# Kernel tuning notes

Measured on AMD Instinct MI355X. Metric: run time of the kernel, lower is better.

The kernel has to match this reference:

```python
import jax, jax.numpy as jnp
import numpy as np
import math

D_MODEL = 512
NHEAD = 8
HEAD = D_MODEL // NHEAD


def _pe(length, d):
    pos = np.arange(length)[:, None].astype(np.float32)
    div = np.exp(np.arange(0, d, 2).astype(np.float32) * (-math.log(10000.0) / d))
    pe = np.zeros((length, d), np.float32)
    pe[:, 0::2] = np.sin(pos * div)
    pe[:, 1::2] = np.cos(pos * div)
    return jnp.asarray(pe)


def _ln(x, g, b, eps=1e-5):
    m = x.mean(-1, keepdims=True)
    v = ((x - m) ** 2).mean(-1, keepdims=True)
    return (x - m) / jnp.sqrt(v + eps) * g + b


def _mha(q_in, k_in, v_in, w_in, b_in, w_out, b_out, mask=None):
    d = q_in.shape[-1]
    wq, wk, wv = jnp.split(w_in, 3, axis=0)
    bq, bk, bv = jnp.split(b_in, 3, axis=0)
    B, Sq, _ = q_in.shape
    Sk = k_in.shape[1]
    q = (q_in @ wq.T + bq).reshape(B, Sq, NHEAD, HEAD)
    k = (k_in @ wk.T + bk).reshape(B, Sk, NHEAD, HEAD)
    v = (v_in @ wv.T + bv).reshape(B, Sk, NHEAD, HEAD)
    s = jnp.einsum('bqhd,bkhd->bhqk', q, k) / math.sqrt(HEAD)
    if mask is not None:
        s = s + mask
    a = jax.nn.softmax(s, axis=-1)
    o = jnp.einsum('bhqk,bkhd->bqhd', a, v).reshape(B, Sq, d)
    return o @ w_out.T + b_out


def setup_inputs() -> dict:
    rng = np.random.default_rng(0)
    def r(*s):
        return jnp.asarray(rng.standard_normal(s, dtype=np.float32) * 0.02)
    L, d, ff, di, do = 6, 512, 2048, 64, 64
    B, S, T = 4, 512, 256
    return dict(
        src=jnp.asarray(rng.standard_normal((B, S, di), dtype=np.float32)),
        tgt=jnp.asarray(rng.standard_normal((B, T, do), dtype=np.float32)),
        enc_in_w=r(d, di), enc_in_b=r(d),
        dec_in_w=r(d, do), dec_in_b=r(d),
        out_w=r(do, d), out_b=r(do),
        enc_attn_w=r(L, 3 * d, d), enc_attn_b=r(L, 3 * d),
        enc_out_w=r(L, d, d), enc_out_b=r(L, d),
        enc_ff1_w=r(L, ff, d), enc_ff1_b=r(L, ff),
        enc_ff2_w=r(L, d, ff), enc_ff2_b=r(L, d),
        enc_ln1_g=jnp.ones((L, d)), enc_ln1_b=jnp.zeros((L, d)),
        enc_ln2_g=jnp.ones((L, d)), enc_ln2_b=jnp.zeros((L, d)),
        dec_sa_w=r(L, 3 * d, d), dec_sa_b=r(L, 3 * d),
        dec_sa_out_w=r(L, d, d), dec_sa_out_b=r(L, d),
        dec_ca_w=r(L, 3 * d, d), dec_ca_b=r(L, 3 * d),
        dec_ca_out_w=r(L, d, d), dec_ca_out_b=r(L, d),
        dec_ff1_w=r(L, ff, d), dec_ff1_b=r(L, ff),
        dec_ff2_w=r(L, d, ff), dec_ff2_b=r(L, d),
        dec_ln1_g=jnp.ones((L, d)), dec_ln1_b=jnp.zeros((L, d)),
        dec_ln2_g=jnp.ones((L, d)), dec_ln2_b=jnp.zeros((L, d)),
        dec_ln3_g=jnp.ones((L, d)), dec_ln3_b=jnp.zeros((L, d)),
    )


def reference(src, tgt, enc_in_w, enc_in_b, dec_in_w, dec_in_b, out_w, out_b,
              enc_attn_w, enc_attn_b, enc_out_w, enc_out_b,
              enc_ff1_w, enc_ff1_b, enc_ff2_w, enc_ff2_b,
              enc_ln1_g, enc_ln1_b, enc_ln2_g, enc_ln2_b,
              dec_sa_w, dec_sa_b, dec_sa_out_w, dec_sa_out_b,
              dec_ca_w, dec_ca_b, dec_ca_out_w, dec_ca_out_b,
              dec_ff1_w, dec_ff1_b, dec_ff2_w, dec_ff2_b,
              dec_ln1_g, dec_ln1_b, dec_ln2_g, dec_ln2_b, dec_ln3_g, dec_ln3_b):
    d = D_MODEL
    sq = math.sqrt(d)
    S, T = src.shape[1], tgt.shape[1]
    L = enc_attn_w.shape[0]
    # encoder: 'cosine' pos encoding (dropout disabled / eval)
    x = (src @ enc_in_w.T + enc_in_b) * sq + _pe(S, d)[None]
    for i in range(L):
        a = _mha(x, x, x, enc_attn_w[i], enc_attn_b[i], enc_out_w[i], enc_out_b[i])
        x = _ln(x + a, enc_ln1_g[i], enc_ln1_b[i])
        f = jax.nn.relu(x @ enc_ff1_w[i].T + enc_ff1_b[i]) @ enc_ff2_w[i].T + enc_ff2_b[i]
        x = _ln(x + f, enc_ln2_g[i], enc_ln2_b[i])
    memory = x
    # decoder: teacher-forced prefix loop == single causal-masked pass.
    # NOTE: original adds pe[0] to EVERY step (pos_encoder on a length-1 slice).
    y = (tgt @ dec_in_w.T + dec_in_b) * sq + _pe(1, d)[0]
    mask = jnp.where(jnp.tril(jnp.ones((T, T), bool)), 0.0, -1e9).astype(y.dtype)
    for i in range(L):
        a = _mha(y, y, y, dec_sa_w[i], dec_sa_b[i], dec_sa_out_w[i], dec_sa_out_b[i], mask)
        y = _ln(y + a, dec_ln1_g[i], dec_ln1_b[i])
        c = _mha(y, memory, memory, dec_ca_w[i], dec_ca_b[i], dec_ca_out_w[i], dec_ca_out_b[i])
        y = _ln(y + c, dec_ln2_g[i], dec_ln2_b[i])
        f = jax.nn.relu(y @ dec_ff1_w[i].T + dec_ff1_b[i]) @ dec_ff2_w[i].T + dec_ff2_b[i]
        y = _ln(y + f, dec_ln3_g[i], dec_ln3_b[i])
    return y @ out_w.T + out_b
```

## Files before the change

kernel.cpp:

```cpp
#include <hip/hip_runtime.h>
#include <hip/hip_bf16.h>
#include <math.h>

#define BB 4
#define SEQ 512
#define TGT 256
#define DM 512
#define FFD 2048
#define NH 8
#define HD 64
#define NL 6

typedef unsigned short u16;
typedef __attribute__((ext_vector_type(4))) float f4;
typedef __attribute__((ext_vector_type(4))) unsigned short us4;
typedef __attribute__((ext_vector_type(8))) unsigned short us8;
typedef __attribute__((ext_vector_type(8))) short s8;

__device__ inline u16 f2b(float f) {
    __hip_bfloat16 h = __float2bfloat16(f);
    return *reinterpret_cast<u16*>(&h);
}
__device__ inline float b2f(u16 u) {
    unsigned int x = ((unsigned int)u) << 16;
    float f;
    __builtin_memcpy(&f, &x, 4);
    return f;
}
__device__ inline us4 cvt4(f4 v) {
    us4 u;
    u.x = f2b(v.x); u.y = f2b(v.y); u.z = f2b(v.z); u.w = f2b(v.w);
    return u;
}

struct CastSegs {
    const float* src[24];
    u16* dst[24];
    int cum[25];
    int nseg;
};

__global__ __launch_bounds__(256) void castseg_k(CastSegs cs)
{
    const int g0 = blockIdx.x << 10;
    int s = 0;
    while (g0 >= cs.cum[s + 1]) s++;
    const f4* __restrict__ sp = (const f4*)cs.src[s];
    us8* __restrict__ dp = (us8*)cs.dst[s];
    const int base = g0 - cs.cum[s] + (int)threadIdx.x;

    f4 lo[4], hi[4];
#pragma unroll
    for (int k = 0; k < 4; k++) {
        size_t g = (size_t)(base + (k << 8));
        lo[k] = sp[g * 2];
        hi[k] = sp[g * 2 + 1];
    }
#pragma unroll
    for (int k = 0; k < 4; k++) {
        us4 ul = cvt4(lo[k]), uh = cvt4(hi[k]);
        us8 o;
#pragma unroll
        for (int e = 0; e < 4; e++) { o[e] = ul[e]; o[e + 4] = uh[e]; }
        dp[base + (k << 8)] = o;
    }
}

__global__ void kvbias_k(const float* __restrict__ dec_ca_b, float* __restrict__ out)
{
    int idx = blockIdx.x * blockDim.x + threadIdx.x;
    if (idx >= NL * 2 * DM) return;
    int layer = idx >> 10, j = idx & 1023;
    out[idx] = dec_ca_b[layer * 3 * DM + DM + j];
}

template <int RELU, int OUTF32, int BM, int PE>
__global__ __launch_bounds__(256) void mgemm_k(
    const u16* __restrict__ A, const u16* __restrict__ W,
    const float* __restrict__ bias, const u16* __restrict__ resid,
    void* __restrict__ Cv, int M, int N, int K, float alpha)
{
    constexpr int MI = BM / 32;
    __shared__ u16 As[2][BM][72];
    __shared__ u16 Bs[2][64][72];
    const int bm = blockIdx.y * BM, bn = blockIdx.x * 64;
    const int tid = threadIdx.x;
    const int wave = tid >> 6, lane = tid & 63;
    const int wr = (wave >> 1) * (BM / 2), wc = (wave & 1) * 32;
    const int lm = lane & 15, quad = lane >> 4;
    const int sbr = tid >> 2, sbc = (tid & 3) * 16;
    const int sar = (BM == 64) ? (tid >> 2) : (tid >> 3);
    const int sac = (BM == 64) ? ((tid & 3) * 16) : ((tid & 7) * 8);

    const u16* Arow = A + (size_t)(bm + sar) * K + sac;
    const u16* Wrow = W + (size_t)(bn + sbr) * K + sbc;

    us8 a0 = *(const us8*)(Arow);
    us8 a1;
    if (BM == 64) a1 = *(const us8*)(Arow + 8);
    us8 b0 = *(const us8*)(Wrow);
    us8 b1 = *(const us8*)(Wrow + 8);

    f4 acc[MI][2];
#pragma unroll
    for (int i = 0; i < MI; i++)
#pragma unroll
        for (int j = 0; j < 2; j++) acc[i][j] = (f4)(0.f);

    const int nk = K >> 6;
    *(us8*)&As[0][sar][sac] = a0;
    if (BM == 64) *(us8*)&As[0][sar][sac + 8] = a1;
    *(us8*)&Bs[0][sbr][sbc] = b0;
    *(us8*)&Bs[0][sbr][sbc + 8] = b1;
    __syncthreads();

    for (int t = 0; t < nk; t++) {
        const int cb = t & 1;
        if (t + 1 < nk) {
            int off = (t + 1) << 6;
            a0 = *(const us8*)(Arow + off);
            if (BM == 64) a1 = *(const us8*)(Arow + off + 8);
            b0 = *(const us8*)(Wrow + off);
            b1 = *(const us8*)(Wrow + off + 8);
        }
#pragma unroll
        for (int ks = 0; ks < 2; ks++) {
            s8 af[MI], bfr[2];
#pragma unroll
            for (int i = 0; i < MI; i++) af[i] = *(const s8*)&As[cb][wr + i * 16 + lm][ks * 32 + quad * 8];
#pragma unroll
            for (int j = 0; j < 2; j++) bfr[j] = *(const s8*)&Bs[cb][wc + j * 16 + lm][ks * 32 + quad * 8];
#pragma unroll
            for (int i = 0; i < MI; i++)
#pragma unroll
                for (int j = 0; j < 2; j++)
                    acc[i][j] = __builtin_amdgcn_mfma_f32_16x16x32_bf16(af[i], bfr[j], acc[i][j], 0, 0, 0);
        }
        if (t + 1 < nk) {
            const int nb = cb ^ 1;
            *(us8*)&As[nb][sar][sac] = a0;
            if (BM == 64) *(us8*)&As[nb][sar][sac + 8] = a1;
            *(us8*)&Bs[nb][sbr][sbc] = b0;
            *(us8*)&Bs[nb][sbr][sbc + 8] = b1;
            __syncthreads();
        }
    }

#pragma unroll
    for (int j = 0; j < 2; j++) {
        int n = bn + wc + j * 16 + lm;
        float bv = bias[n];
        float dv = 0.f;
        if (PE == 1) dv = expf((float)(n & ~1) * (-9.210340371976184f / (float)DM));
#pragma unroll
        for (int i = 0; i < MI; i++) {
#pragma unroll
            for (int r = 0; r < 4; r++) {
                int m = bm + wr + i * 16 + quad * 4 + r;
                float v = (acc[i][j][r] + bv) * alpha;
                if (PE == 1) {
                    float ang = (float)(m & (SEQ - 1)) * dv;
                    v += (n & 1) ? cosf(ang) : sinf(ang);
                }
                if (PE == 2) { if (n & 1) v += 1.f; }
                if (RELU) v = fmaxf(v, 0.f);
                size_t off = (size_t)m * N + n;
                if (resid) v += b2f(resid[off]);
                if (OUTF32) ((float*)Cv)[off] = v;
                else        ((u16*)Cv)[off]  = f2b(v);
            }
        }
    }
}

template <int RELU>
__global__ __launch_bounds__(256) void mgemm128_k(
    const u16* __restrict__ A, const u16* __restrict__ W,
    const float* __restrict__ bias, u16* __restrict__ C,
    int M, int N, int K)
{
    __shared__ u16 As[2][64][72];
    __shared__ u16 Bs[2][128][72];
    const int bm = blockIdx.y * 64, bn = blockIdx.x * 128;
    const int tid = threadIdx.x;
    const int wave = tid >> 6, lane = tid & 63;
    const int wr = (wave >> 1) * 32, wc = (wave & 1) * 64;
    const int lm = lane & 15, quad = lane >> 4;
    const int sar = tid >> 2, sac = (tid & 3) * 16;
    const int sbr = tid >> 1, sbc = (tid & 1) * 32;

    const u16* Arow = A + (size_t)(bm + sar) * K + sac;
    const u16* Wrow = W + (size_t)(bn + sbr) * K + sbc;

    us8 a0 = *(const us8*)(Arow);
    us8 a1 = *(const us8*)(Arow + 8);
    us8 b0 = *(const us8*)(Wrow);
    us8 b1 = *(const us8*)(Wrow + 8);
    us8 b2 = *(const us8*)(Wrow + 16);
    us8 b3 = *(const us8*)(Wrow + 24);

    f4 acc[2][4];
#pragma unroll
    for (int i = 0; i < 2; i++)
#pragma unroll
        for (int j = 0; j < 4; j++) acc[i][j] = (f4)(0.f);

    const int nk = K >> 6;
    *(us8*)&As[0][sar][sac]     = a0;
    *(us8*)&As[0][sar][sac + 8] = a1;
    *(us8*)&Bs[0][sbr][sbc]      = b0;
    *(us8*)&Bs[0][sbr][sbc + 8]  = b1;
    *(us8*)&Bs[0][sbr][sbc + 16] = b2;
    *(us8*)&Bs[0][sbr][sbc + 24] = b3;
    __syncthreads();

    for (int t = 0; t < nk; t++) {
        const int cb = t & 1;
        if (t + 1 < nk) {
            int off = (t + 1) << 6;
            a0 = *(const us8*)(Arow + off);
            a1 = *(const us8*)(Arow + off + 8);
            b0 = *(const us8*)(Wrow + off);
            b1 = *(const us8*)(Wrow + off + 8);
            b2 = *(const us8*)(Wrow + off + 16);
            b3 = *(const us8*)(Wrow + off + 24);
        }
#pragma unroll
        for (int ks = 0; ks < 2; ks++) {
            s8 af[2], bfr[4];
#pragma unroll
            for (int i = 0; i < 2; i++) af[i] = *(const s8*)&As[cb][wr + i * 16 + lm][ks * 32 + quad * 8];
#pragma unroll
            for (int j = 0; j < 4; j++) bfr[j] = *(const s8*)&Bs[cb][wc + j * 16 + lm][ks * 32 + quad * 8];
#pragma unroll
            for (int i = 0; i < 2; i++)
#pragma unroll
                for (int j = 0; j < 4; j++)
                    acc[i][j] = __builtin_amdgcn_mfma_f32_16x16x32_bf16(af[i], bfr[j], acc[i][j], 0, 0, 0);
        }
        if (t + 1 < nk) {
            const int nb = cb ^ 1;
            *(us8*)&As[nb][sar][sac]     = a0;
            *(us8*)&As[nb][sar][sac + 8] = a1;
            *(us8*)&Bs[nb][sbr][sbc]      = b0;
            *(us8*)&Bs[nb][sbr][sbc + 8]  = b1;
            *(us8*)&Bs[nb][sbr][sbc + 16] = b2;
            *(us8*)&Bs[nb][sbr][sbc + 24] = b3;
            __syncthreads();
        }
    }

#pragma unroll
    for (int j = 0; j < 4; j++) {
        int n = bn + wc + j * 16 + lm;
        float bv = bias[n];
#pragma unroll
        for (int i = 0; i < 2; i++) {
#pragma unroll
            for (int r = 0; r < 4; r++) {
                int m = bm + wr + i * 16 + quad * 4 + r;
                float v = acc[i][j][r] + bv;
                if (RELU) v = fmaxf(v, 0.f);
                C[(size_t)m * N + n] = f2b(v);
            }
        }
    }
}

template <int CAUSAL>
__global__ __launch_bounds__(256) void flash_k(
    const u16* __restrict__ Q, int qs,
    const u16* __restrict__ Kp, int ks,
    const u16* __restrict__ V, int vs,
    u16* __restrict__ O, int Sq, int Sk)
{
    __shared__ u16 Qs[64][72];
    __shared__ u16 Ks[128][72];
    __shared__ u16 Vs[64][136];
    __shared__ u16 Ps[4][16][136];
    const int bm = blockIdx.x * 64;
    const int bh = blockIdx.y, b = bh >> 3, h = bh & 7;
    const int tid = threadIdx.x;
    const int wave = tid >> 6, lane = tid & 63;
    const int lm = lane & 15, quad = lane >> 4;

    const u16* Qb = Q + (size_t)(b * Sq + bm) * qs + h * HD;
    {
        int r = tid >> 2, c = (tid & 3) * 16;
        *(us8*)&Qs[r][c]     = *(const us8*)(Qb + (size_t)r * qs + c);
        *(us8*)&Qs[r][c + 8] = *(const us8*)(Qb + (size_t)r * qs + c + 8);
    }

    float mrow[4], lrow[4];
    f4 o[4];
#pragma unroll
    for (int r = 0; r < 4; r++) { mrow[r] = -1e30f; lrow[r] = 0.f; }
#pragma unroll
    for (int nt = 0; nt < 4; nt++) o[nt] = (f4)(0.f);

    const u16* Kb = Kp + (size_t)(b * Sk) * ks + h * HD;
    const u16* Vb = V + (size_t)(b * Sk) * vs + h * HD;
    int nkt = Sk >> 7;
    if (CAUSAL) { int lim = (bm + 63) / 128 + 1; if (lim < nkt) nkt = lim; }

    const int vd = tid & 63, vkb = tid >> 6;
    const int kr = tid >> 3, kc8 = (tid & 7) * 8;

    for (int kt = 0; kt < nkt; kt++) {
        const u16* Kt = Kb + ((size_t)kt << 7) * ks;
        const u16* Vt = Vb + ((size_t)kt << 7) * vs;
#pragma unroll
        for (int p = 0; p < 4; p++) {
            int r = p * 32 + kr;
            *(us8*)&Ks[r][kc8] = *(const us8*)(Kt + (size_t)r * ks + kc8);
        }
#pragma unroll
        for (int p = 0; p < 32; p++) {
            int kv = p * 4 + vkb;
            Vs[vd][kv] = Vt[(size_t)kv * vs + vd];
        }
        __syncthreads();

        f4 sa[8];
#pragma unroll
        for (int nt = 0; nt < 8; nt++) sa[nt] = (f4)(0.f);
#pragma unroll
        for (int ks2 = 0; ks2 < 2; ks2++) {
            s8 aq = *(const s8*)&Qs[wave * 16 + lm][ks2 * 32 + quad * 8];
#pragma unroll
            for (int nt = 0; nt < 8; nt++) {
                s8 bk = *(const s8*)&Ks[nt * 16 + lm][ks2 * 32 + quad * 8];
                sa[nt] = __builtin_amdgcn_mfma_f32_16x16x32_bf16(aq, bk, sa[nt], 0, 0, 0);
            }
        }
        float tmx[4] = {-1e30f, -1e30f, -1e30f, -1e30f};
#pragma unroll
        for (int nt = 0; nt < 8; nt++) {
#pragma unroll
            for (int r = 0; r < 4; r++) {
                float v = sa[nt][r] * 0.125f;
                if (CAUSAL) {
                    int col = (kt << 7) + nt * 16 + lm;
                    int row = bm + wave * 16 + quad * 4 + r;
                    if (col > row) v = -1e30f;
                }
                sa[nt][r] = v;
                tmx[r] = fmaxf(tmx[r], v);
            }
        }
#pragma unroll
        for (int st = 1; st < 16; st <<= 1)
#pragma unroll
            for (int r = 0; r < 4; r++) tmx[r] = fmaxf(tmx[r], __shfl_xor(tmx[r], st));
        float al[4];
#pragma unroll
        for (int r = 0; r < 4; r++) {
            float mn = fmaxf(mrow[r], tmx[r]);
            al[r] = __expf(mrow[r] - mn);
            mrow[r] = mn;
        }
        float ts[4] = {0.f, 0.f, 0.f, 0.f};
#pragma unroll
        for (int nt = 0; nt < 8; nt++) {
#pragma unroll
            for (int r = 0; r < 4; r++) {
                float pe = __expf(sa[nt][r] - mrow[r]);
                sa[nt][r] = pe;
                ts[r] += pe;
            }
        }
#pragma unroll
        for (int st = 1; st < 16; st <<= 1)
#pragma unroll
            for (int r = 0; r < 4; r++) ts[r] += __shfl_xor(ts[r], st);
#pragma unroll
        for (int r = 0; r < 4; r++) lrow[r] = lrow[r] * al[r] + ts[r];
#pragma unroll
        for (int nt = 0; nt < 4; nt++)
#pragma unroll
            for (int r = 0; r < 4; r++) o[nt][r] *= al[r];
#pragma unroll
        for (int nt = 0; nt < 8; nt++)
#pragma unroll
            for (int r = 0; r < 4; r++)
                Ps[wave][quad * 4 + r][nt * 16 + lm] = f2b(sa[nt][r]);
#pragma unroll
        for (int kc = 0; kc < 4; kc++) {
            s8 ap = *(const s8*)&Ps[wave][lm][kc * 32 + quad * 8];
#pragma unroll
            for (int nt = 0; nt < 4; nt++) {
                s8 bv = *(const s8*)&Vs[nt * 16 + lm][kc * 32 + quad * 8];
                o[nt] = __builtin_amdgcn_mfma_f32_16x16x32_bf16(ap, bv, o[nt], 0, 0, 0);
            }
        }
        __syncthreads();
    }

    float inv[4];
#pragma unroll
    for (int r = 0; r < 4; r++) inv[r] = 1.f / lrow[r];
#pragma unroll
    for (int nt = 0; nt < 4; nt++) {
#pragma unroll
        for (int r = 0; r < 4; r++) {
            int m = bm + wave * 16 + quad * 4 + r;
            O[(size_t)(b * Sq + m) * DM + h * HD + nt * 16 + lm] = f2b(o[nt][r] * inv[r]);
        }
    }
}

__global__ __launch_bounds__(256) void ln_k(u16* __restrict__ x,
                                            const float* __restrict__ g,
                                            const float* __restrict__ b)
{
    const int wave = threadIdx.x >> 6, lane = threadIdx.x & 63;
    const int row = blockIdx.x * 4 + wave;
    u16* xr = x + (size_t)row * DM + lane * 8;
    us8 v8 = *(const us8*)xr;
    float v[8];
    float s = 0.f;
#pragma unroll
    for (int e = 0; e < 8; e++) { v[e] = b2f(v8[e]); s += v[e]; }
#pragma unroll
    for (int st = 1; st < 64; st <<= 1) s += __shfl_xor(s, st);
    float mean = s * (1.f / DM);
    float q = 0.f;
#pragma unroll
    for (int e = 0; e < 8; e++) { float d = v[e] - mean; q += d * d; }
#pragma unroll
    for (int st = 1; st < 64; st <<= 1) q += __shfl_xor(q, st);
    float rstd = rsqrtf(q * (1.f / DM) + 1e-5f);
    f4 g0 = *(const f4*)(g + lane * 8), g1 = *(const f4*)(g + lane * 8 + 4);
    f4 b0 = *(const f4*)(b + lane * 8), b1 = *(const f4*)(b + lane * 8 + 4);
    us8 o;
#pragma unroll
    for (int e = 0; e < 4; e++) {
        o[e]     = f2b((v[e]     - mean) * rstd * g0[e] + b0[e]);
        o[e + 4] = f2b((v[e + 4] - mean) * rstd * g1[e] + b1[e]);
    }
    *(us8*)xr = o;
}

static inline dim3 mg64(int M, int N) { return dim3(N / 64, M / 64); }
static inline dim3 mg32(int M, int N) { return dim3(N / 64, M / 32); }
static inline dim3 mg128(int M, int N) { return dim3(N / 128, M / 64); }

extern "C" void kernel_launch(void* const* d_in, const int* in_sizes, int n_in,
                              void* d_out, int out_size, void* d_ws, size_t ws_size,
                              hipStream_t stream)
{
    const float* src       = (const float*)d_in[0];
    const float* tgt       = (const float*)d_in[1];
    const float* enc_in_w  = (const float*)d_in[2];
    const float* enc_in_b  = (const float*)d_in[3];
    const float* dec_in_w  = (const float*)d_in[4];
    const float* dec_in_b  = (const float*)d_in[5];
    const float* out_w     = (const float*)d_in[6];
    const float* out_b     = (const float*)d_in[7];
    const float* enc_attn_w = (const float*)d_in[8];
    const float* enc_attn_b = (const float*)d_in[9];
    const float* enc_out_w  = (const float*)d_in[10];
    const float* enc_out_b  = (const float*)d_in[11];
    const float* enc_ff1_w  = (const float*)d_in[12];
    const float* enc_ff1_b  = (const float*)d_in[13];
    const float* enc_ff2_w  = (const float*)d_in[14];
    const float* enc_ff2_b  = (const float*)d_in[15];
    const float* enc_ln1_g  = (const float*)d_in[16];
    const float* enc_ln1_b  = (const float*)d_in[17];
    const float* enc_ln2_g  = (const float*)d_in[18];
    const float* enc_ln2_b  = (const float*)d_in[19];
    const float* dec_sa_w     = (const float*)d_in[20];
    const float* dec_sa_b     = (const float*)d_in[21];
    const float* dec_sa_out_w = (const float*)d_in[22];
    const float* dec_sa_out_b = (const float*)d_in[23];
    const float* dec_ca_w     = (const float*)d_in[24];
    const float* dec_ca_b     = (const float*)d_in[25];
    const float* dec_ca_out_w = (const float*)d_in[26];
    const float* dec_ca_out_b = (const float*)d_in[27];
    const float* dec_ff1_w    = (const float*)d_in[28];
    const float* dec_ff1_b    = (const float*)d_in[29];
    const float* dec_ff2_w    = (const float*)d_in[30];
    const float* dec_ff2_b    = (const float*)d_in[31];
    const float* dec_ln1_g    = (const float*)d_in[32];
    const float* dec_ln1_b    = (const float*)d_in[33];
    const float* dec_ln2_g    = (const float*)d_in[34];
    const float* dec_ln2_b    = (const float*)d_in[35];
    const float* dec_ln3_g    = (const float*)d_in[36];
    const float* dec_ln3_b    = (const float*)d_in[37];

    const int ME = BB * SEQ;
    const int MD = BB * TGT;
    const int BH = BB * NH;
    const float SQD = 22.627416997969522f;

    const size_t SZ_ATTN = (size_t)NL * 3 * DM * DM;
    const size_t SZ_OUT  = (size_t)NL * DM * DM;
    const size_t SZ_FF   = (size_t)NL * FFD * DM;

    float* fp = (float*)d_ws;
    float* kvbias = fp; fp += NL * 2 * DM;
    u16* p = (u16*)fp;
    u16* xa   = p; p += (size_t)ME * DM;
    u16* xb   = p; p += (size_t)ME * DM;
    u16* reg1 = p; p += (size_t)ME * FFD;
    u16* tbuf = p; p += (size_t)ME * DM;
    u16* ya   = p; p += (size_t)MD * DM;
    u16* yb   = p; p += (size_t)MD * DM;
    u16* kvall = p; p += (size_t)ME * NL * 2 * DM;
    u16* src_b     = p; p += (size_t)ME * HD;
    u16* tgt_b     = p; p += (size_t)MD * HD;
    u16* enc_in_wb = p; p += (size_t)DM * HD;
    u16* dec_in_wb = p; p += (size_t)DM * HD;
    u16* out_wb    = p; p += (size_t)HD * DM;
    u16* enc_at_wb = p; p += SZ_ATTN;
    u16* enc_ow_wb = p; p += SZ_OUT;
    u16* enc_f1_wb = p; p += SZ_FF;
    u16* enc_f2_wb = p; p += SZ_FF;
    u16* dec_sa_wb = p; p += SZ_ATTN;
    u16* dec_sao_wb = p; p += SZ_OUT;
    u16* dec_ca_wb = p; p += SZ_ATTN;
    u16* dec_cao_wb = p; p += SZ_OUT;
    u16* dec_f1_wb = p; p += SZ_FF;
    u16* dec_f2_wb = p; p += SZ_FF;
    u16* kvstack   = p; p += (size_t)NL * 2 * DM * DM;

    CastSegs cs;
    int ns = 0;
    auto seg = [&](const float* s, u16* d, size_t n) {
        cs.src[ns] = s; cs.dst[ns] = d;
        cs.cum[ns + 1] = cs.cum[ns] + (int)(n / 8);
        ns++;
    };
    cs.cum[0] = 0;
    seg(src,          src_b,     (size_t)ME * HD);
    seg(tgt,          tgt_b,     (size_t)MD * HD);
    seg(enc_in_w,     enc_in_wb, (size_t)DM * HD);
    seg(dec_in_w,     dec_in_wb, (size_t)DM * HD);
    seg(out_w,        out_wb,    (size_t)HD * DM);
    seg(enc_attn_w,   enc_at_wb, SZ_ATTN);
    seg(enc_out_w,    enc_ow_wb, SZ_OUT);
    seg(enc_ff1_w,    enc_f1_wb, SZ_FF);
    seg(enc_ff2_w,    enc_f2_wb, SZ_FF);
    seg(dec_sa_w,     dec_sa_wb, SZ_ATTN);
    seg(dec_sa_out_w, dec_sao_wb, SZ_OUT);
    seg(dec_ca_w,     dec_ca_wb, SZ_ATTN);
    seg(dec_ca_out_w, dec_cao_wb, SZ_OUT);
    seg(dec_ff1_w,    dec_f1_wb, SZ_FF);
    seg(dec_ff2_w,    dec_f2_wb, SZ_FF);
    for (int i = 0; i < NL; i++)
        seg(dec_ca_w + (size_t)i * 3 * DM * DM + (size_t)DM * DM,
            kvstack + (size_t)i * 2 * DM * DM, (size_t)2 * DM * DM);
    cs.nseg = ns;
    castseg_k<<<cs.cum[ns] >> 10, 256, 0, stream>>>(cs);
    kvbias_k<<<(NL * 2 * DM + 255) / 256, 256, 0, stream>>>(dec_ca_b, kvbias);

    mgemm_k<0, 0, 64, 1><<<mg64(ME, DM), 256, 0, stream>>>(src_b, enc_in_wb, enc_in_b, nullptr, xa, ME, DM, HD, SQD);

    u16* cur = xa; u16* alt = xb;
    for (int i = 0; i < NL; i++) {
        const u16* W = enc_at_wb + (size_t)i * 3 * DM * DM;
        const float* Bw = enc_attn_b + (size_t)i * 3 * DM;
        mgemm128_k<0><<<mg128(ME, 3 * DM), 256, 0, stream>>>(cur, W, Bw, reg1, ME, 3 * DM, DM);
        flash_k<0><<<dim3(SEQ / 64, BH), 256, 0, stream>>>(reg1, 3 * DM, reg1 + DM, 3 * DM, reg1 + 2 * DM, 3 * DM, tbuf, SEQ, SEQ);
        mgemm_k<0, 0, 32, 0><<<mg32(ME, DM), 256, 0, stream>>>(tbuf, enc_ow_wb + (size_t)i * DM * DM, enc_out_b + (size_t)i * DM, cur, alt, ME, DM, DM, 1.f);
        ln_k<<<ME / 4, 256, 0, stream>>>(alt, enc_ln1_g + (size_t)i * DM, enc_ln1_b + (size_t)i * DM);
        { u16* t = cur; cur = alt; alt = t; }
        mgemm128_k<1><<<mg128(ME, FFD), 256, 0, stream>>>(cur, enc_f1_wb + (size_t)i * FFD * DM, enc_ff1_b + (size_t)i * FFD, reg1, ME, FFD, DM);
        mgemm_k<0, 0, 32, 0><<<mg32(ME, DM), 256, 0, stream>>>(reg1, enc_f2_wb + (size_t)i * DM * FFD, enc_ff2_b + (size_t)i * DM, cur, alt, ME, DM, FFD, 1.f);
        ln_k<<<ME / 4, 256, 0, stream>>>(alt, enc_ln2_g + (size_t)i * DM, enc_ln2_b + (size_t)i * DM);
        { u16* t = cur; cur = alt; alt = t; }
    }
    u16* mem = cur;

    mgemm128_k<0><<<mg128(ME, NL * 2 * DM), 256, 0, stream>>>(mem, kvstack, kvbias, kvall, ME, NL * 2 * DM, DM);

    mgemm_k<0, 0, 32, 2><<<mg32(MD, DM), 256, 0, stream>>>(tgt_b, dec_in_wb, dec_in_b, nullptr, ya, MD, DM, HD, SQD);

    u16* dc = ya; u16* da = yb;
    for (int i = 0; i < NL; i++) {
        const u16* W = dec_sa_wb + (size_t)i * 3 * DM * DM;
        const float* Bw = dec_sa_b + (size_t)i * 3 * DM;
        mgemm128_k<0><<<mg128(MD, 3 * DM), 256, 0, stream>>>(dc, W, Bw, reg1, MD, 3 * DM, DM);
        flash_k<1><<<dim3(TGT / 64, BH), 256, 0, stream>>>(reg1, 3 * DM, reg1 + DM, 3 * DM, reg1 + 2 * DM, 3 * DM, tbuf, TGT, TGT);
        mgemm_k<0, 0, 32, 0><<<mg32(MD, DM), 256, 0, stream>>>(tbuf, dec_sao_wb + (size_t)i * DM * DM, dec_sa_out_b + (size_t)i * DM, dc, da, MD, DM, DM, 1.f);
        ln_k<<<MD / 4, 256, 0, stream>>>(da, dec_ln1_g + (size_t)i * DM, dec_ln1_b + (size_t)i * DM);
        { u16* t = dc; dc = da; da = t; }

        const u16* Wc = dec_ca_wb + (size_t)i * 3 * DM * DM;
        const float* Bc = dec_ca_b + (size_t)i * 3 * DM;
        u16* qbuf = reg1;
        mgemm_k<0, 0, 32, 0><<<mg32(MD, DM), 256, 0, stream>>>(dc, Wc, Bc, nullptr, qbuf, MD, DM, DM, 1.f);
        const u16* kvl = kvall + (size_t)i * 2 * DM;
        flash_k<0><<<dim3(TGT / 64, BH), 256, 0, stream>>>(qbuf, DM, kvl, NL * 2 * DM, kvl + DM, NL * 2 * DM, tbuf, TGT, SEQ);
        mgemm_k<0, 0, 32, 0><<<mg32(MD, DM), 256, 0, stream>>>(tbuf, dec_cao_wb + (size_t)i * DM * DM, dec_ca_out_b + (size_t)i * DM, dc, da, MD, DM, DM, 1.f);
        ln_k<<<MD / 4, 256, 0, stream>>>(da, dec_ln2_g + (size_t)i * DM, dec_ln2_b + (size_t)i * DM);
        { u16* t = dc; dc = da; da = t; }

        mgemm128_k<1><<<mg128(MD, FFD), 256, 0, stream>>>(dc, dec_f1_wb + (size_t)i * FFD * DM, dec_ff1_b + (size_t)i * FFD, reg1, MD, FFD, DM);
        mgemm_k<0, 0, 32, 0><<<mg32(MD, DM), 256, 0, stream>>>(reg1, dec_f2_wb + (size_t)i * DM * FFD, dec_ff2_b + (size_t)i * DM, dc, da, MD, DM, FFD, 1.f);
        ln_k<<<MD / 4, 256, 0, stream>>>(da, dec_ln3_g + (size_t)i * DM, dec_ln3_b + (size_t)i * DM);
        { u16* t = dc; dc = da; da = t; }
    }

    mgemm_k<0, 1, 32, 0><<<mg32(MD, HD), 256, 0, stream>>>(dc, out_wb, out_b, nullptr, (float*)d_out, MD, HD, DM, 1.f);
}
```

Before: 1.263 ms.

## Fuse attention out-projection with residual LayerNorm; drop KV weight re-cast copy

Adds a full-row GEMM kernel (32 rows x 512 columns per block, 512 threads) that computes the attention output projection, adds bias and residual, and applies LayerNorm in its epilogue. This replaces the separate GEMM plus ln_k pair for the encoder self-attention and both decoder attention sublayers, removing one kernel launch and one activation round trip per sublayer. The cross-attention KV GEMM now reads K/V weights straight from the cast decoder weights via a row-index remap, so the duplicate kvstack cast is gone. The cast kernel is reworked to move 4 elements per thread-item with 8 items per thread. The fused kernel has only 64 blocks for the encoder and 32 for the decoder, which may under-fill the GPU. It also computes variance as E[x^2]-mean^2 in fp32.

```diff
diff --git a/kernel.cpp b/kernel.cpp
--- a/kernel.cpp
+++ b/kernel.cpp
@@ -12,6 +12,7 @@
 #define NL 6
 
 typedef unsigned short u16;
+typedef __attribute__((ext_vector_type(2))) unsigned short us2;
 typedef __attribute__((ext_vector_type(4))) float f4;
 typedef __attribute__((ext_vector_type(4))) unsigned short us4;
 typedef __attribute__((ext_vector_type(8))) unsigned short us8;
@@ -42,28 +43,18 @@
 
 __global__ __launch_bounds__(256) void castseg_k(CastSegs cs)
 {
-    const int g0 = blockIdx.x << 10;
+    const int g0 = blockIdx.x << 11;
     int s = 0;
     while (g0 >= cs.cum[s + 1]) s++;
     const f4* __restrict__ sp = (const f4*)cs.src[s];
-    us8* __restrict__ dp = (us8*)cs.dst[s];
+    us4* __restrict__ dp = (us4*)cs.dst[s];
     const int base = g0 - cs.cum[s] + (int)threadIdx.x;
 
-    f4 lo[4], hi[4];
-#pragma unroll
-    for (int k = 0; k < 4; k++) {
-        size_t g = (size_t)(base + (k << 8));
-        lo[k] = sp[g * 2];
-        hi[k] = sp[g * 2 + 1];
-    }
-#pragma unroll
-    for (int k = 0; k < 4; k++) {
-        us4 ul = cvt4(lo[k]), uh = cvt4(hi[k]);
-        us8 o;
-#pragma unroll
-        for (int e = 0; e < 4; e++) { o[e] = ul[e]; o[e + 4] = uh[e]; }
-        dp[base + (k << 8)] = o;
-    }
+    f4 v[8];
+#pragma unroll
+    for (int k = 0; k < 8; k++) v[k] = sp[base + (k << 8)];
+#pragma unroll
+    for (int k = 0; k < 8; k++) dp[base + (k << 8)] = cvt4(v[k]);
 }
 
 __global__ void kvbias_k(const float* __restrict__ dec_ca_b, float* __restrict__ out)
@@ -173,7 +164,7 @@
     }
 }
 
-template <int RELU>
+template <int RELU, int KVMAP>
 __global__ __launch_bounds__(256) void mgemm128_k(
     const u16* __restrict__ A, const u16* __restrict__ W,
     const float* __restrict__ bias, u16* __restrict__ C,
@@ -189,8 +180,11 @@
     const int sar = tid >> 2, sac = (tid & 3) * 16;
     const int sbr = tid >> 1, sbc = (tid & 1) * 32;
 
+    int brow = bn + sbr;
+    if (KVMAP) brow = (brow >> 10) * (3 * DM) + DM + (brow & 1023);
+
     const u16* Arow = A + (size_t)(bm + sar) * K + sac;
-    const u16* Wrow = W + (size_t)(bn + sbr) * K + sbc;
+    const u16* Wrow = W + (size_t)brow * K + sbc;
 
     us8 a0 = *(const us8*)(Arow);
     us8 a1 = *(const us8*)(Arow + 8);
@@ -262,6 +256,139 @@
                 float v = acc[i][j][r] + bv;
                 if (RELU) v = fmaxf(v, 0.f);
                 C[(size_t)m * N + n] = f2b(v);
+            }
+        }
+    }
+}
+
+__global__ __launch_bounds__(512) void mgemmln_k(
+    const u16* __restrict__ A, const u16* __restrict__ W,
+    const float* __restrict__ bias, const u16* __restrict__ resid,
+    const float* __restrict__ g, const float* __restrict__ b,
+    u16* __restrict__ C, int M, int K)
+{
+    __shared__ u16 As[32][40];
+    __shared__ u16 Bs[512][40];
+    __shared__ float ps[8][32], pq[8][32];
+    const int bm = blockIdx.x * 32;
+    const int tid = threadIdx.x;
+    const int wave = tid >> 6, lane = tid & 63;
+    const int wc = wave * 64;
+    const int lm = lane & 15, quad = lane >> 4;
+
+    const int sar = tid >> 4, sac = (tid & 15) * 2;
+    const int sbr = tid >> 1, sbc = (tid & 1) * 16;
+
+    const u16* Ap  = A + (size_t)(bm + sar) * K + sac;
+    const u16* Wp0 = W + (size_t)sbr * K + sbc;
+    const u16* Wp1 = W + (size_t)(sbr + 256) * K + sbc;
+
+    us2 a0 = *(const us2*)Ap;
+    us8 rb00 = *(const us8*)(Wp0);
+    us8 rb01 = *(const us8*)(Wp0 + 8);
+    us8 rb10 = *(const us8*)(Wp1);
+    us8 rb11 = *(const us8*)(Wp1 + 8);
+
+    f4 acc[2][4];
+#pragma unroll
+    for (int i = 0; i < 2; i++)
+#pragma unroll
+        for (int j = 0; j < 4; j++) acc[i][j] = (f4)(0.f);
+
+    const int nk = K >> 5;
+    for (int t = 0; t < nk; t++) {
+        if (t) __syncthreads();
+        *(us2*)&As[sar][sac] = a0;
+        *(us8*)&Bs[sbr][sbc]           = rb00;
+        *(us8*)&Bs[sbr][sbc + 8]       = rb01;
+        *(us8*)&Bs[sbr + 256][sbc]     = rb10;
+        *(us8*)&Bs[sbr + 256][sbc + 8] = rb11;
+        __syncthreads();
+        if (t + 1 < nk) {
+            int off = (t + 1) << 5;
+            a0   = *(const us2*)(Ap + off);
+            rb00 = *(const us8*)(Wp0 + off);
+            rb01 = *(const us8*)(Wp0 + off + 8);
+            rb10 = *(const us8*)(Wp1 + off);
+            rb11 = *(const us8*)(Wp1 + off + 8);
+        }
+        s8 af0 = *(const s8*)&As[lm][quad * 8];
+        s8 af1 = *(const s8*)&As[16 + lm][quad * 8];
+#pragma unroll
+        for (int j = 0; j < 4; j++) {
+            s8 bf = *(const s8*)&Bs[wc + j * 16 + lm][quad * 8];
+            acc[0][j] = __builtin_amdgcn_mfma_f32_16x16x32_bf16(af0, bf, acc[0][j], 0, 0, 0);
+            acc[1][j] = __builtin_amdgcn_mfma_f32_16x16x32_bf16(af1, bf, acc[1][j], 0, 0, 0);
+        }
+    }
+
+    float rs[2][4], rq[2][4];
+#pragma unroll
+    for (int i = 0; i < 2; i++)
+#pragma unroll
+        for (int r = 0; r < 4; r++) { rs[i][r] = 0.f; rq[i][r] = 0.f; }
+#pragma unroll
+    for (int j = 0; j < 4; j++) {
+        int n = wc + j * 16 + lm;
+        float bv = bias[n];
+#pragma unroll
+        for (int i = 0; i < 2; i++) {
+#pragma unroll
+            for (int r = 0; r < 4; r++) {
+                int m = bm + i * 16 + quad * 4 + r;
+                float v = acc[i][j][r] + bv + b2f(resid[(size_t)m * DM + n]);
+                acc[i][j][r] = v;
+                rs[i][r] += v;
+                rq[i][r] += v * v;
+            }
+        }
+    }
+#pragma unroll
+    for (int st = 1; st < 16; st <<= 1) {
+#pragma unroll
+        for (int i = 0; i < 2; i++)
+#pragma unroll
+            for (int r = 0; r < 4; r++) {
+                rs[i][r] += __shfl_xor(rs[i][r], st);
+                rq[i][r] += __shfl_xor(rq[i][r], st);
+            }
+    }
+    if (lm == 0) {
+#pragma unroll
+        for (int i = 0; i < 2; i++)
+#pragma unroll
+            for (int r = 0; r < 4; r++) {
+                int row = i * 16 + quad * 4 + r;
+                ps[wave][row] = rs[i][r];
+                pq[wave][row] = rq[i][r];
+            }
+    }
+    __syncthreads();
+    float mu[2][4], rsd[2][4];
+#pragma unroll
+    for (int i = 0; i < 2; i++) {
+#pragma unroll
+        for (int r = 0; r < 4; r++) {
+            int row = i * 16 + quad * 4 + r;
+            float S = 0.f, Q = 0.f;
+#pragma unroll
+            for (int w = 0; w < 8; w++) { S += ps[w][row]; Q += pq[w][row]; }
+            float mean = S * (1.f / DM);
+            float var = Q * (1.f / DM) - mean * mean;
+            mu[i][r] = mean;
+            rsd[i][r] = rsqrtf(var + 1e-5f);
+        }
+    }
+#pragma unroll
+    for (int j = 0; j < 4; j++) {
+        int n = wc + j * 16 + lm;
+        float gv = g[n], bv2 = b[n];
+#pragma unroll
+        for (int i = 0; i < 2; i++) {
+#pragma unroll
+            for (int r = 0; r < 4; r++) {
+                int m = bm + i * 16 + quad * 4 + r;
+                C[(size_t)m * DM + n] = f2b((acc[i][j][r] - mu[i][r]) * rsd[i][r] * gv + bv2);
             }
         }
     }
@@ -522,13 +649,12 @@
     u16* dec_cao_wb = p; p += SZ_OUT;
     u16* dec_f1_wb = p; p += SZ_FF;
     u16* dec_f2_wb = p; p += SZ_FF;
-    u16* kvstack   = p; p += (size_t)NL * 2 * DM * DM;
 
     CastSegs cs;
     int ns = 0;
     auto seg = [&](const float* s, u16* d, size_t n) {
         cs.src[ns] = s; cs.dst[ns] = d;
-        cs.cum[ns + 1] = cs.cum[ns] + (int)(n / 8);
+        cs.cum[ns + 1] = cs.cum[ns] + (int)(n / 4);
         ns++;
     };
     cs.cum[0] = 0;
@@ -547,11 +673,8 @@
     seg(dec_ca_out_w, dec_cao_wb, SZ_OUT);
     seg(dec_ff1_w,    dec_f1_wb, SZ_FF);
     seg(dec_ff2_w,    dec_f2_wb, SZ_FF);
-    for (int i = 0; i < NL; i++)
-        seg(dec_ca_w + (size_t)i * 3 * DM * DM + (size_t)DM * DM,
-            kvstack + (size_t)i * 2 * DM * DM, (size_t)2 * DM * DM);
     cs.nseg = ns;
-    castseg_k<<<cs.cum[ns] >> 10, 256, 0, stream>>>(cs);
+    castseg_k<<<cs.cum[ns] >> 11, 256, 0, stream>>>(cs);
     kvbias_k<<<(NL * 2 * DM + 255) / 256, 256, 0, stream>>>(dec_ca_b, kvbias);
 
     mgemm_k<0, 0, 64, 1><<<mg64(ME, DM), 256, 0, stream>>>(src_b, enc_in_wb, enc_in_b, nullptr, xa, ME, DM, HD, SQD);
@@ -560,19 +683,19 @@
     for (int i = 0; i < NL; i++) {
         const u16* W = enc_at_wb + (size_t)i * 3 * DM * DM;
         const float* Bw = enc_attn_b + (size_t)i * 3 * DM;
-        mgemm128_k<0><<<mg128(ME, 3 * DM), 256, 0, stream>>>(cur, W, Bw, reg1, ME, 3 * DM, DM);
+        mgemm128_k<0, 0><<<mg128(ME, 3 * DM), 256, 0, stream>>>(cur, W, Bw, reg1, ME, 3 * DM, DM);
         flash_k<0><<<dim3(SEQ / 64, BH), 256, 0, stream>>>(reg1, 3 * DM, reg1 + DM, 3 * DM, reg1 + 2 * DM, 3 * DM, tbuf, SEQ, SEQ);
-        mgemm_k<0, 0, 32, 0><<<mg32(ME, DM), 256, 0, stream>>>(tbuf, enc_ow_wb + (size_t)i * DM * DM, enc_out_b + (size_t)i * DM, cur, alt, ME, DM, DM, 1.f);
-        ln_k<<<ME / 4, 256, 0, stream>>>(alt, enc_ln1_g + (size_t)i * DM, enc_ln1_b + (size_t)i * DM);
+        mgemmln_k<<<ME / 32, 512, 0, stream>>>(tbuf, enc_ow_wb + (size_t)i * DM * DM, enc_out_b + (size_t)i * DM,
+                                               cur, enc_ln1_g + (size_t)i * DM, enc_ln1_b + (size_t)i * DM, alt, ME, DM);
         { u16* t = cur; cur = alt; alt = t; }
-        mgemm128_k<1><<<mg128(ME, FFD), 256, 0, stream>>>(cur, enc_f1_wb + (size_t)i * FFD * DM, enc_ff1_b + (size_t)i * FFD, reg1, ME, FFD, DM);
+        mgemm128_k<1, 0><<<mg128(ME, FFD), 256, 0, stream>>>(cur, enc_f1_wb + (size_t)i * FFD * DM, enc_ff1_b + (size_t)i * FFD, reg1, ME, FFD, DM);
         mgemm_k<0, 0, 32, 0><<<mg32(ME, DM), 256, 0, stream>>>(reg1, enc_f2_wb + (size_t)i * DM * FFD, enc_ff2_b + (size_t)i * DM, cur, alt, ME, DM, FFD, 1.f);
         ln_k<<<ME / 4, 256, 0, stream>>>(alt, enc_ln2_g + (size_t)i * DM, enc_ln2_b + (size_t)i * DM);
         { u16* t = cur; cur = alt; alt = t; }
     }
     u16* mem = cur;
 
-    mgemm128_k<0><<<mg128(ME, NL * 2 * DM), 256, 0, stream>>>(mem, kvstack, kvbias, kvall, ME, NL * 2 * DM, DM);
+    mgemm128_k<0, 1><<<mg128(ME, NL * 2 * DM), 256, 0, stream>>>(mem, dec_ca_wb, kvbias, kvall, ME, NL * 2 * DM, DM);
 
     mgemm_k<0, 0, 32, 2><<<mg32(MD, DM), 256, 0, stream>>>(tgt_b, dec_in_wb, dec_in_b, nullptr, ya, MD, DM, HD, SQD);
 
@@ -580,10 +703,10 @@
     for (int i = 0; i < NL; i++) {
         const u16* W = dec_sa_wb + (size_t)i * 3 * DM * DM;
         const float* Bw = dec_sa_b + (size_t)i * 3 * DM;
-        mgemm128_k<0><<<mg128(MD, 3 * DM), 256, 0, stream>>>(dc, W, Bw, reg1, MD, 3 * DM, DM);
+        mgemm128_k<0, 0><<<mg128(MD, 3 * DM), 256, 0, stream>>>(dc, W, Bw, reg1, MD, 3 * DM, DM);
         flash_k<1><<<dim3(TGT / 64, BH), 256, 0, stream>>>(reg1, 3 * DM, reg1 + DM, 3 * DM, reg1 + 2 * DM, 3 * DM, tbuf, TGT, TGT);
-        mgemm_k<0, 0, 32, 0><<<mg32(MD, DM), 256, 0, stream>>>(tbuf, dec_sao_wb + (size_t)i * DM * DM, dec_sa_out_b + (size_t)i * DM, dc, da, MD, DM, DM, 1.f);
-        ln_k<<<MD / 4, 256, 0, stream>>>(da, dec_ln1_g + (size_t)i * DM, dec_ln1_b + (size_t)i * DM);
+        mgemmln_k<<<MD / 32, 512, 0, stream>>>(tbuf, dec_sao_wb + (size_t)i * DM * DM, dec_sa_out_b + (size_t)i * DM,
+                                               dc, dec_ln1_g + (size_t)i * DM, dec_ln1_b + (size_t)i * DM, da, MD, DM);
         { u16* t = dc; dc = da; da = t; }
 
         const u16* Wc = dec_ca_wb + (size_t)i * 3 * DM * DM;
@@ -592,11 +715,11 @@
         mgemm_k<0, 0, 32, 0><<<mg32(MD, DM), 256, 0, stream>>>(dc, Wc, Bc, nullptr, qbuf, MD, DM, DM, 1.f);
         const u16* kvl = kvall + (size_t)i * 2 * DM;
         flash_k<0><<<dim3(TGT / 64, BH), 256, 0, stream>>>(qbuf, DM, kvl, NL * 2 * DM, kvl + DM, NL * 2 * DM, tbuf, TGT, SEQ);
-        mgemm_k<0, 0, 32, 0><<<mg32(MD, DM), 256, 0, stream>>>(tbuf, dec_cao_wb + (size_t)i * DM * DM, dec_ca_out_b + (size_t)i * DM, dc, da, MD, DM, DM, 1.f);
-        ln_k<<<MD / 4, 256, 0, stream>>>(da, dec_ln2_g + (size_t)i * DM, dec_ln2_b + (size_t)i * DM);
+        mgemmln_k<<<MD / 32, 512, 0, stream>>>(tbuf, dec_cao_wb + (size_t)i * DM * DM, dec_ca_out_b + (size_t)i * DM,
+                                               dc, dec_ln2_g + (size_t)i * DM, dec_ln2_b + (size_t)i * DM, da, MD, DM);
         { u16* t = dc; dc = da; da = t; }
 
-        mgemm128_k<1><<<mg128(MD, FFD), 256, 0, stream>>>(dc, dec_f1_wb + (size_t)i * FFD * DM, dec_ff1_b + (size_t)i * FFD, reg1, MD, FFD, DM);
+        mgemm128_k<1, 0><<<mg128(MD, FFD), 256, 0, stream>>>(dc, dec_f1_wb + (size_t)i * FFD * DM, dec_ff1_b + (size_t)i * FFD, reg1, MD, FFD, DM);
         mgemm_k<0, 0, 32, 0><<<mg32(MD, DM), 256, 0, stream>>>(reg1, dec_f2_wb + (size_t)i * DM * FFD, dec_ff2_b + (size_t)i * DM, dc, da, MD, DM, FFD, 1.f);
         ln_k<<<MD / 4, 256, 0, stream>>>(da, dec_ln3_g + (size_t)i * DM, dec_ln3_b + (size_t)i * DM);
         { u16* t = dc; dc = da; da = t; }
```

After: 1.393 ms. +10.3%, slower.
